# Kernel tuning notes

Measured on AMD Instinct MI355X. Metric: run time of the kernel, lower is better.

The kernel has to match this reference:

```python
import jax, jax.numpy as jnp
import numpy as np
from jax import lax

DEPTH = 8
LEAK = 0.01  # activations.relu(x, 0.01) == leaky relu


def _lrelu(z):
    return jnp.where(z >= 0, z, LEAK * z)


def _forward(x, mask, bucket_size, W_emb, b_emb, W, U, b, W1, b1,
             W_action_1, U_action_1, b_action_1, W_action_3, b_action_3):
    S = int(bucket_size)
    B = x.shape[0]
    H = W_emb.shape[1]
    dm = mask.T[:S]                         # [S,B] data mask (float)
    xe = x @ W_emb + b_emb                  # [B,S,H] embedding
    xe = jnp.transpose(xe, (1, 0, 2))[:S]   # [S,B,H] time-major
    # last_value_mask: 1 only at the final time step
    lvm = jnp.concatenate([jnp.zeros((S - 1, B), jnp.float32),
                           jnp.ones((1, B), jnp.float32)], axis=0)

    def hstep(carry, seq):
        h_tm1, nm_tm1, hv_tm1 = carry
        xt, pm, phv, lv = seq
        # action MLP -> per-sample gate
        a = _lrelu(xt @ W_action_1 + h_tm1 @ U_action_1 + b_action_1)  # [B,A]
        nm = jnp.clip(0.2 * (a @ W_action_3 + b_action_3) + 0.5, 0.0, 1.0)[:, 0]  # hard_sigmoid
        nm = (1.0 - lv) * (pm * phv * nm)
        both = pm * phv * (1.0 - nm) * hv_tm1
        x_only = pm * phv * (nm + (1.0 - nm) * (1.0 - hv_tm1))
        h_only = (1.0 - pm + pm * (1.0 - phv)) * (1.0 - nm) * hv_tm1
        hv = both + x_only + h_only
        h_ = _lrelu(xt @ W + h_tm1 @ U + b)      # [B,inner]
        h_ = _lrelu(h_ @ W1 + b1)                # [B,H]
        h = both[:, None] * h_ + x_only[:, None] * xt + h_only[:, None] * h_tm1
        return (h, nm, hv), (h, nm, hv)

    def vstep(carry, _):
        xv, xm, phv = carry  # [S,B,H], [S,B], [S,B]
        init = (jnp.zeros((B, H), jnp.float32),
                jnp.ones((B,), jnp.float32),
                jnp.zeros((B,), jnp.float32))
        _, (hs, nms, hvs) = lax.scan(hstep, init, (xv, xm, phv, lvm))
        # shift new_mask left by one step, pad last step with ones
        nms = jnp.concatenate([nms[1:], jnp.ones((1, B), jnp.float32)], axis=0)
        return (hs, nms, hvs), None

    (hfin, _, _), _ = lax.scan(vstep, (xe, dm, dm), None, length=DEPTH - 1)
    return hfin[-1]  # [B,H]: last time step of the last vertical level


def setup_inputs() -> dict:
    key = jax.random.key(0)
    ks = jax.random.split(key, 9)
    B, S, IN, H, INNER, A = 64, 256, 256, 256, 512, 64
    g = lambda k, shp: jax.random.normal(k, shp, jnp.float32) * np.float32(np.sqrt(2.0 / (shp[0] + shp[1])))
    return {
        "x": jax.random.normal(ks[0], (B, S, IN), jnp.float32),
        "mask": jnp.ones((B, S), jnp.float32),
        "bucket_size": S,
        "W_emb": g(ks[1], (IN, H)),
        "b_emb": jnp.zeros((H,), jnp.float32),
        "W": g(ks[2], (H, INNER)),
        "U": g(ks[3], (H, INNER)),
        "b": jnp.zeros((INNER,), jnp.float32),
        "W1": g(ks[4], (INNER, H)),
        "b1": jnp.zeros((H,), jnp.float32),
        "W_action_1": g(ks[5], (H, A)),
        "U_action_1": g(ks[6], (H, A)),
        "b_action_1": jnp.zeros((A,), jnp.float32),
        "W_action_3": g(ks[7], (A, 1)),
        "b_action_3": jnp.zeros((1,), jnp.float32),
    }


def reference(x, mask, bucket_size, W_emb, b_emb, W, U, b, W1, b1,
              W_action_1, U_action_1, b_action_1, W_action_3, b_action_3):
    return _forward(x, mask, bucket_size, W_emb, b_emb, W, U, b, W1, b1,
                    W_action_1, U_action_1, b_action_1, W_action_3, b_action_3)
```

## Files before the change

kernel.cpp:

```cpp
#include <hip/hip_runtime.h>
#include <stdint.h>


typedef _Float16 f16x8 __attribute__((ext_vector_type(8)));
typedef float    f32x4 __attribute__((ext_vector_type(4)));

static constexpr int SS = 256, BB = 64, DIN = 256, DH = 256, DNN = 512, DA = 64;

static constexpr size_t OFF_FLAGS = 0;
static constexpr size_t OFF_WEMB  = 8192;
static constexpr size_t SZ_WEMB   = (size_t)DIN * DH * 2;
static constexpr size_t OFF_W     = OFF_WEMB + SZ_WEMB;
static constexpr size_t SZ_WU     = (size_t)DH * DNN * 2;
static constexpr size_t OFF_U     = OFF_W + SZ_WU;
static constexpr size_t OFF_W1    = OFF_U + SZ_WU;
static constexpr size_t SZ_W1     = (size_t)DNN * DH * 2;
static constexpr size_t OFF_WA1   = OFF_W1 + SZ_W1;
static constexpr size_t SZ_WA     = (size_t)DH * DA * 2;
static constexpr size_t OFF_UA1   = OFF_WA1 + SZ_WA;
static constexpr size_t OFF_NM    = OFF_UA1 + SZ_WA;
static constexpr size_t SZ_NM     = (size_t)SS * BB * 4;
static constexpr size_t OFF_HV    = OFF_NM + 8 * SZ_NM;
static constexpr size_t OFF_G1    = OFF_HV + 8 * SZ_NM;
static constexpr size_t SZ_G1     = (size_t)BB * DNN * 2;
static constexpr size_t OFF_Z     = OFF_G1 + 8 * SZ_G1;
static constexpr size_t OFF_HB    = (size_t)4 << 20;
static constexpr size_t SZ_HB     = (size_t)SS * BB * DH * 2;
static constexpr size_t WS_NEEDED = OFF_HB + 8 * SZ_HB;

__device__ __forceinline__ float lrelu(float v) { return v >= 0.0f ? v : 0.01f * v; }

__device__ __forceinline__ f32x4 ld128(const f32x4* p) {
  f32x4 r;
  asm volatile("global_load_dwordx4 %0, %1, off sc0 sc1" : "=v"(r) : "v"(p) : "memory");
  return r;
}
__device__ __forceinline__ void st128(f32x4* p, f32x4 v) {
  asm volatile("global_store_dwordx4 %0, %1, off sc0 sc1" :: "v"(p), "v"(v) : "memory");
}
__device__ __forceinline__ float ldf(const float* p) {
  float r;
  asm volatile("global_load_dword %0, %1, off sc0 sc1" : "=v"(r) : "v"(p) : "memory");
  return r;
}
__device__ __forceinline__ void stf(float* p, float v) {
  asm volatile("global_store_dword %0, %1, off sc0 sc1" :: "v"(p), "v"(v) : "memory");
}
__device__ __forceinline__ void vwait() { asm volatile("s_waitcnt vmcnt(0)" ::: "memory"); }

__device__ __forceinline__ void pollf(const unsigned* p, unsigned need) {
  #pragma nounroll
  for (int g = 0; g < (1 << 18); ++g) {
    unsigned v;
    asm volatile("global_load_dword %0, %1, off sc0 sc1\n\ts_waitcnt vmcnt(0)"
                 : "=v"(v) : "v"(p) : "memory");
    if (v >= need) return;
  }
}

__global__ void zero_flags_k(unsigned* f) {
  f[threadIdx.x] = 0u;
  f[threadIdx.x + 1024] = 0u;
}

__global__ void pack_weight_k(const float* __restrict__ src, _Float16* __restrict__ dst,
                              int K, int N) {
  int idx = blockIdx.x * 256 + threadIdx.x;
  if (idx >= K * N) return;
  int k = idx / N, n = idx - k * N;
  int kt = k >> 5, q = (k >> 3) & 3, jj = k & 7;
  int nt = n >> 4, l = n & 15;
  size_t p = (((size_t)(kt * (N >> 4) + nt) * 4 + q) * 16 + l) * 8 + jj;
  dst[p] = (_Float16)src[idx];
}

__global__ __launch_bounds__(512, 2) void emb_k(const float* __restrict__ xin,
                                                const float* __restrict__ b_emb,
                                                char* __restrict__ ws) {
  const int tid = threadIdx.x, wave = tid >> 6, lane = tid & 63;
  const int l15 = lane & 15, quad = lane >> 4;
  const _Float16* Wp = (const _Float16*)(ws + OFF_WEMB);
  _Float16* xe = (_Float16*)(ws + OFF_HB);

  f16x8 bE[16];
  #pragma unroll
  for (int kt = 0; kt < 8; ++kt)
    #pragma unroll
    for (int i = 0; i < 2; ++i)
      bE[kt * 2 + i] = *(const f16x8*)(Wp + (((size_t)(kt * 16 + (wave * 2 + i)) * 4 + quad) * 16 + l15) * 8);
  float ber[2] = { b_emb[(wave * 2) * 16 + l15], b_emb[(wave * 2 + 1) * 16 + l15] };

  __shared__ __align__(16) _Float16 xtF[32 * 65 * 8];
  __shared__ __align__(16) _Float16 oF[32 * 65 * 8];

  for (int tt = 0; tt < 4; ++tt) {
    const int t = (int)blockIdx.x + 64 * tt;
    #pragma unroll
    for (int c = 0; c < 4; ++c) {
      int u = tid + 512 * c, s = u >> 5, kg = u & 31;
      const float* src = xin + ((size_t)s * SS + t) * DIN + kg * 8;
      f32x4 v0 = *(const f32x4*)src, v1 = *(const f32x4*)(src + 4);
      f16x8 p;
      p[0]=(_Float16)v0[0]; p[1]=(_Float16)v0[1]; p[2]=(_Float16)v0[2]; p[3]=(_Float16)v0[3];
      p[4]=(_Float16)v1[0]; p[5]=(_Float16)v1[1]; p[6]=(_Float16)v1[2]; p[7]=(_Float16)v1[3];
      *(f16x8*)(xtF + ((size_t)kg * 65 + s) * 8) = p;
    }
    __syncthreads();
    f32x4 acc[2][4] = {};
    #pragma unroll
    for (int kt = 0; kt < 8; ++kt) {
      f16x8 ax[4];
      #pragma unroll
      for (int mt = 0; mt < 4; ++mt)
        ax[mt] = *(const f16x8*)(xtF + (((size_t)(kt * 4 + quad)) * 65 + (mt * 16 + l15)) * 8);
      #pragma unroll
      for (int i = 0; i < 2; ++i)
        #pragma unroll
        for (int mt = 0; mt < 4; ++mt)
          acc[i][mt] = __builtin_amdgcn_mfma_f32_16x16x32_f16(ax[mt], bE[kt * 2 + i], acc[i][mt], 0, 0, 0);
    }
    #pragma unroll
    for (int i = 0; i < 2; ++i) {
      int n = (wave * 2 + i) * 16 + l15;
      int kq = n >> 3, jn = n & 7;
      #pragma unroll
      for (int mt = 0; mt < 4; ++mt)
        #pragma unroll
        for (int r = 0; r < 4; ++r) {
          int s = mt * 16 + quad * 4 + r;
          oF[((size_t)kq * 65 + s) * 8 + jn] = (_Float16)(acc[i][mt][r] + ber[i]);
        }
    }
    __syncthreads();
    #pragma unroll
    for (int c = 0; c < 4; ++c) {
      int u = tid + 512 * c, kq = u >> 6, s = u & 63;
      f32x4 v = *(const f32x4*)(oF + ((size_t)kq * 65 + s) * 8);
      *((f32x4*)(xe + (((size_t)t * 32 + kq) * 64 + s) * 8)) = v;
    }
    __syncthreads();
  }
}

__global__ __launch_bounds__(512, 2) void pipe_k(
    const float* __restrict__ mask, const float* __restrict__ b_in,
    const float* __restrict__ b1v, const float* __restrict__ bA1,
    const float* __restrict__ WA3, const float* __restrict__ bA3,
    char* __restrict__ ws, float* __restrict__ outp) {
  const int level = 1 + ((int)blockIdx.x >> 3);
  const int j     = (int)blockIdx.x & 7;
  const int tid   = threadIdx.x, wave = tid >> 6, lane = tid & 63;
  const int l15   = lane & 15, quad = lane >> 4;

  unsigned* flags = (unsigned*)(ws + OFF_FLAGS);
  unsigned* hfl   = flags + level * 64;
  unsigned* hflP  = flags + (level - 1) * 64;
  unsigned* gfl   = flags + (8 + level) * 64;

  const _Float16* Wp   = (const _Float16*)(ws + OFF_W);
  const _Float16* Up   = (const _Float16*)(ws + OFF_U);
  const _Float16* W1p  = (const _Float16*)(ws + OFF_W1);
  const _Float16* WA1p = (const _Float16*)(ws + OFF_WA1);
  const _Float16* UA1p = (const _Float16*)(ws + OFF_UA1);

  const f32x4* hPrev4 = (const f32x4*)((_Float16*)(ws + OFF_HB) + (size_t)(level - 1) * SS * BB * DH);
  f32x4*       hOwn4  = (f32x4*)((_Float16*)(ws + OFF_HB) + (size_t)level * SS * BB * DH);
  f32x4*       g1g4   = (f32x4*)(ws + OFF_G1 + (size_t)level * SZ_G1);
  float*       zg     = (float*)(ws + OFF_Z + (size_t)level * 4096);
  float*       nmW    = (float*)(ws + OFF_NM + (size_t)level * SZ_NM);
  float*       hvW    = (float*)(ws + OFF_HV + (size_t)level * SZ_NM);
  const float* nmR    = (const float*)(ws + OFF_NM + (size_t)(level - 1) * SZ_NM);
  const float* hvR    = (const float*)(ws + OFF_HV + (size_t)(level - 1) * SZ_NM);

  const int ntG = j * 4 + (wave >> 1);
  const int m0  = (wave & 1) * 2;
  f16x8 bW[8], bU[8];
  #pragma unroll
  for (int kt = 0; kt < 8; ++kt) {
    bW[kt] = *(const f16x8*)(Wp + (((size_t)(kt * 32 + ntG) * 4 + quad) * 16 + l15) * 8);
    bU[kt] = *(const f16x8*)(Up + (((size_t)(kt * 32 + ntG) * 4 + quad) * 16 + l15) * 8);
  }
  const int nt1 = j * 2 + (wave & 1);
  const int mt1 = wave >> 1;
  f16x8 b1f[16];
  #pragma unroll
  for (int kt = 0; kt < 16; ++kt)
    b1f[kt] = *(const f16x8*)(W1p + (((size_t)(kt * 16 + nt1) * 4 + quad) * 16 + l15) * 8);

  const int nG = ntG * 16 + l15;
  const int nC = nt1 * 16 + l15;
  const float bir  = b_in[nG];
  const float b1r  = b1v[nC];
  const float wa3r = WA3[(j & 3) * 16 + l15];
  const float ba1r = bA1[(j & 3) * 16 + l15];
  const float bA3v = bA3[0];

  __shared__ __align__(16) _Float16 xtF[32 * 64 * 8];
  __shared__ __align__(16) _Float16 htF[32 * 64 * 8];
  __shared__ __align__(16) _Float16 g1F[64 * 64 * 8];
  __shared__ __align__(16) _Float16 waF[16 * 64 * 8];
  __shared__ float gB[64], gX[64], gH[64], gHv[64];

  if (j < 4) {
    for (int u = tid; u < 1024; u += 512) {
      int ktm = u >> 6, lu = u & 63, kt = ktm >> 1, m = ktm & 1;
      const _Float16* sp = (m ? UA1p : WA1p) +
          (((size_t)(kt * 4 + j) * 4 + (lu >> 4)) * 16 + (lu & 15)) * 8;
      *(f16x8*)(waF + (size_t)u * 8) = *(const f16x8*)sp;
    }
  }
  for (int i = tid; i < 32 * 64 * 8; i += 512) htF[i] = (_Float16)0;
  if (tid < 64) gHv[tid] = 0.0f;
  float hreg[4] = {0.f, 0.f, 0.f, 0.f};
  __syncthreads();

  if (level >= 2) pollf(hflP + wave, 1);
  __syncthreads();
  {
    f32x4 pf[4];
    #pragma unroll
    for (int c = 0; c < 4; ++c) pf[c] = ld128(hPrev4 + tid + 512 * c);
    vwait();
    #pragma unroll
    for (int c = 0; c < 4; ++c) ((f32x4*)xtF)[tid + 512 * c] = pf[c];
  }
  __syncthreads();

  for (int t = 0; t < SS; ++t) {
    const bool last = (t == SS - 1);

    if (t > 0) pollf(hfl + wave, (unsigned)t);
    if (level >= 2) {
      unsigned need = (unsigned)((t + 2 <= SS) ? (t + 2) : SS);
      pollf(hflP + wave, need);
    }
    if (t > 0 && wave != j) {
      const f32x4* src = hOwn4 + (size_t)(t - 1) * 2048 + wave * 256;
      f32x4 hv4[4];
      #pragma unroll
      for (int it = 0; it < 4; ++it) hv4[it] = ld128(src + it * 64 + lane);
      vwait();
      #pragma unroll
      for (int it = 0; it < 4; ++it) ((f32x4*)htF)[wave * 256 + it * 64 + lane] = hv4[it];
    }
    __syncthreads();

    {
      f32x4 a0 = {}, a1 = {};
      #pragma unroll
      for (int kt = 0; kt < 8; ++kt) {
        int kq = kt * 4 + quad;
        f16x8 ax0 = *(const f16x8*)(xtF + ((size_t)(kq * 64 + m0 * 16 + l15)) * 8);
        f16x8 ax1 = *(const f16x8*)(xtF + ((size_t)(kq * 64 + (m0 + 1) * 16 + l15)) * 8);
        f16x8 ah0 = *(const f16x8*)(htF + ((size_t)(kq * 64 + m0 * 16 + l15)) * 8);
        f16x8 ah1 = *(const f16x8*)(htF + ((size_t)(kq * 64 + (m0 + 1) * 16 + l15)) * 8);
        a0 = __builtin_amdgcn_mfma_f32_16x16x32_f16(ax0, bW[kt], a0, 0, 0, 0);
        a1 = __builtin_amdgcn_mfma_f32_16x16x32_f16(ax1, bW[kt], a1, 0, 0, 0);
        a0 = __builtin_amdgcn_mfma_f32_16x16x32_f16(ah0, bU[kt], a0, 0, 0, 0);
        a1 = __builtin_amdgcn_mfma_f32_16x16x32_f16(ah1, bU[kt], a1, 0, 0, 0);
      }
      const int kqn = nG >> 3, jn = nG & 7;
      #pragma unroll
      for (int r = 0; r < 4; ++r) {
        g1F[((size_t)kqn * 64 + (m0 * 16 + quad * 4 + r)) * 8 + jn]       = (_Float16)lrelu(a0[r] + bir);
        g1F[((size_t)kqn * 64 + ((m0 + 1) * 16 + quad * 4 + r)) * 8 + jn] = (_Float16)lrelu(a1[r] + bir);
      }
      if (j < 4 && wave < 4) {
        f32x4 aa = {};
        #pragma unroll
        for (int kt = 0; kt < 8; ++kt) {
          int kq = kt * 4 + quad;
          f16x8 ax = *(const f16x8*)(xtF + ((size_t)(kq * 64 + wave * 16 + l15)) * 8);
          f16x8 ah = *(const f16x8*)(htF + ((size_t)(kq * 64 + wave * 16 + l15)) * 8);
          f16x8 bWa = *(const f16x8*)(waF + ((size_t)(kt * 2) * 64 + lane) * 8);
          f16x8 bUa = *(const f16x8*)(waF + ((size_t)(kt * 2 + 1) * 64 + lane) * 8);
          aa = __builtin_amdgcn_mfma_f32_16x16x32_f16(ax, bWa, aa, 0, 0, 0);
          aa = __builtin_amdgcn_mfma_f32_16x16x32_f16(ah, bUa, aa, 0, 0, 0);
        }
        #pragma unroll
        for (int r = 0; r < 4; ++r) {
          float v = lrelu(aa[r] + ba1r) * wa3r;
          v += __shfl_xor(v, 1); v += __shfl_xor(v, 2);
          v += __shfl_xor(v, 4); v += __shfl_xor(v, 8);
          if (l15 == 0) stf(&zg[j * 64 + wave * 16 + quad * 4 + r], v);
        }
      }
    }
    __syncthreads();
    {
      f32x4 v = ((const f32x4*)g1F)[j * 512 + tid];
      st128(g1g4 + j * 512 + tid, v);
      vwait();
    }
    __syncthreads();
    if (tid == 0)
      __hip_atomic_store(gfl + j, (unsigned)(t + 1), __ATOMIC_RELEASE, __HIP_MEMORY_SCOPE_AGENT);

    f32x4 pf[4];
    if (!last) {
      const f32x4* xs = hPrev4 + (size_t)(t + 1) * 2048;
      #pragma unroll
      for (int c = 0; c < 4; ++c) pf[c] = ld128(xs + tid + 512 * c);
      vwait();
    }

    if (wave != j) {
      pollf(gfl + wave, (unsigned)(t + 1));
      const f32x4* src = g1g4 + wave * 512;
      f32x4 g4[8];
      #pragma unroll
      for (int it = 0; it < 8; ++it) g4[it] = ld128(src + it * 64 + lane);
      vwait();
      #pragma unroll
      for (int it = 0; it < 8; ++it) ((f32x4*)g1F)[wave * 512 + it * 64 + lane] = g4[it];
    }
    __syncthreads();

    if (tid < 64) {
      int s = tid;
      float z0 = ldf(zg + s), z1 = ldf(zg + 64 + s), z2 = ldf(zg + 128 + s), z3 = ldf(zg + 192 + s);
      float pm, phv;
      if (level == 1) {
        vwait();
        float mv = mask[(size_t)s * SS + t];
        pm = mv; phv = mv;
      } else {
        size_t tn = (t + 1 < SS) ? (size_t)(t + 1) : 0;
        float pmv = ldf(nmR + tn * BB + s);
        float ph  = ldf(hvR + (size_t)t * BB + s);
        vwait();
        pm  = (t + 1 < SS) ? pmv : 1.0f;
        phv = ph;
      }
      float z    = bA3v + z0 + z1 + z2 + z3;
      float nm0  = fminf(fmaxf(0.2f * z + 0.5f, 0.0f), 1.0f);
      float lv   = last ? 1.0f : 0.0f;
      float nm   = (1.0f - lv) * (pm * phv * nm0);
      float hvp  = gHv[s], omn = 1.0f - nm;
      float both = pm * phv * omn * hvp;
      float xo   = pm * phv * (nm + omn * (1.0f - hvp));
      float ho   = (1.0f - pm * phv) * omn * hvp;
      float hv   = both + xo + ho;
      gB[s] = both; gX[s] = xo; gH[s] = ho; gHv[s] = hv;
      if (j == 0 && level < 7) {
        stf(&nmW[(size_t)t * BB + s], nm);
        stf(&hvW[(size_t)t * BB + s], hv);
      }
    }
    f32x4 c1 = {};
    #pragma unroll
    for (int kt = 0; kt < 16; ++kt) {
      f16x8 ag = *(const f16x8*)(g1F + ((size_t)((kt * 4 + quad) * 64 + mt1 * 16 + l15)) * 8);
      c1 = __builtin_amdgcn_mfma_f32_16x16x32_f16(ag, b1f[kt], c1, 0, 0, 0);
    }
    __syncthreads();

    {
      const int kqc = nC >> 3, jc = nC & 7;
      #pragma unroll
      for (int r = 0; r < 4; ++r) {
        int s = mt1 * 16 + quad * 4 + r;
        float h1  = lrelu(c1[r] + b1r);
        float xtv = (float)xtF[((size_t)(kqc * 64 + s)) * 8 + jc];
        float hn  = gB[s] * h1 + gX[s] * xtv + gH[s] * hreg[r];
        hreg[r] = hn;
        htF[((size_t)(kqc * 64 + s)) * 8 + jc] = (_Float16)hn;
        if (level == 7 && last) outp[(size_t)s * DH + nC] = hn;
      }
    }
    __syncthreads();
    if (tid < 256) {
      f32x4 v = ((const f32x4*)htF)[j * 256 + tid];
      st128(hOwn4 + (size_t)t * 2048 + j * 256 + tid, v);
    }
    if (!last) {
      #pragma unroll
      for (int c = 0; c < 4; ++c) ((f32x4*)xtF)[tid + 512 * c] = pf[c];
    }
    vwait();
    __syncthreads();
    if (tid == 0)
      __hip_atomic_store(hfl + j, (unsigned)(t + 1), __ATOMIC_RELEASE, __HIP_MEMORY_SCOPE_AGENT);
  }
}

extern "C" void kernel_launch(void* const* d_in, const int* in_sizes, int n_in,
                              void* d_out, int out_size, void* d_ws, size_t ws_size,
                              hipStream_t stream) {
  const float* x     = (const float*)d_in[0];
  const float* mask  = (const float*)d_in[1];
  const float* W_emb = (const float*)d_in[3];
  const float* b_emb = (const float*)d_in[4];
  const float* W     = (const float*)d_in[5];
  const float* U     = (const float*)d_in[6];
  const float* b     = (const float*)d_in[7];
  const float* W1    = (const float*)d_in[8];
  const float* b1    = (const float*)d_in[9];
  const float* WA1   = (const float*)d_in[10];
  const float* UA1   = (const float*)d_in[11];
  const float* bA1   = (const float*)d_in[12];
  const float* WA3   = (const float*)d_in[13];
  const float* bA3   = (const float*)d_in[14];
  char* ws = (char*)d_ws;

  if (ws_size < WS_NEEDED) return;

  zero_flags_k<<<1, 1024, 0, stream>>>((unsigned*)(ws + OFF_FLAGS));
  pack_weight_k<<<(DIN * DH + 255) / 256, 256, 0, stream>>>(W_emb, (_Float16*)(ws + OFF_WEMB), DIN, DH);
  pack_weight_k<<<(DH * DNN + 255) / 256, 256, 0, stream>>>(W, (_Float16*)(ws + OFF_W), DH, DNN);
  pack_weight_k<<<(DH * DNN + 255) / 256, 256, 0, stream>>>(U, (_Float16*)(ws + OFF_U), DH, DNN);
  pack_weight_k<<<(DNN * DH + 255) / 256, 256, 0, stream>>>(W1, (_Float16*)(ws + OFF_W1), DNN, DH);
  pack_weight_k<<<(DH * DA + 255) / 256, 256, 0, stream>>>(WA1, (_Float16*)(ws + OFF_WA1), DH, DA);
  pack_weight_k<<<(DH * DA + 255) / 256, 256, 0, stream>>>(UA1, (_Float16*)(ws + OFF_UA1), DH, DA);

  emb_k<<<64, 512, 0, stream>>>(x, b_emb, ws);
  pipe_k<<<56, 512, 0, stream>>>(mask, b, b1, bA1, WA3, bA3, ws, (float*)d_out);
}
```

Before: 3.598 ms.

## Restructure recurrent pipeline to make the full hidden state local and cut cross-block syncs

Each block now computes the entire W1 projection for all 256 hidden columns, with the first GEMM split over two K halves reduced through LDS. Every block therefore holds the full h_t locally, and the per-step exchange of hidden slices between the 8 blocks of a level goes away. Only the g1 activations and the action logits are still exchanged, through double-buffered global scratch, so one global flag handshake per step is removed. The next x_t is prefetched with global_load_lds DMA into ping-pong LDS buffers, and the mask is pre-transposed for coalesced loads. In exchange each block does 8x redundant W1 MFMA work and holds more registers, which adds compute and register pressure.

```diff
diff --git a/kernel.cpp b/kernel.cpp
--- a/kernel.cpp
+++ b/kernel.cpp
@@ -4,26 +4,24 @@
 
 typedef _Float16 f16x8 __attribute__((ext_vector_type(8)));
 typedef float    f32x4 __attribute__((ext_vector_type(4)));
+typedef unsigned int u32;
 
 static constexpr int SS = 256, BB = 64, DIN = 256, DH = 256, DNN = 512, DA = 64;
 
 static constexpr size_t OFF_FLAGS = 0;
-static constexpr size_t OFF_WEMB  = 8192;
-static constexpr size_t SZ_WEMB   = (size_t)DIN * DH * 2;
-static constexpr size_t OFF_W     = OFF_WEMB + SZ_WEMB;
-static constexpr size_t SZ_WU     = (size_t)DH * DNN * 2;
-static constexpr size_t OFF_U     = OFF_W + SZ_WU;
-static constexpr size_t OFF_W1    = OFF_U + SZ_WU;
-static constexpr size_t SZ_W1     = (size_t)DNN * DH * 2;
-static constexpr size_t OFF_WA1   = OFF_W1 + SZ_W1;
-static constexpr size_t SZ_WA     = (size_t)DH * DA * 2;
-static constexpr size_t OFF_UA1   = OFF_WA1 + SZ_WA;
-static constexpr size_t OFF_NM    = OFF_UA1 + SZ_WA;
+static constexpr size_t OFF_MASKT = 8192;
+static constexpr size_t OFF_WEMB  = OFF_MASKT + 65536;
+static constexpr size_t OFF_W     = OFF_WEMB + (size_t)DIN * DH * 2;
+static constexpr size_t OFF_U     = OFF_W + (size_t)DH * DNN * 2;
+static constexpr size_t OFF_W1    = OFF_U + (size_t)DH * DNN * 2;
+static constexpr size_t OFF_WA1   = OFF_W1 + (size_t)DNN * DH * 2;
+static constexpr size_t OFF_UA1   = OFF_WA1 + (size_t)DH * DA * 2;
+static constexpr size_t OFF_NM    = OFF_UA1 + (size_t)DH * DA * 2;
 static constexpr size_t SZ_NM     = (size_t)SS * BB * 4;
 static constexpr size_t OFF_HV    = OFF_NM + 8 * SZ_NM;
 static constexpr size_t OFF_G1    = OFF_HV + 8 * SZ_NM;
 static constexpr size_t SZ_G1     = (size_t)BB * DNN * 2;
-static constexpr size_t OFF_Z     = OFF_G1 + 8 * SZ_G1;
+static constexpr size_t OFF_Z     = OFF_G1 + 8 * 2 * SZ_G1;
 static constexpr size_t OFF_HB    = (size_t)4 << 20;
 static constexpr size_t SZ_HB     = (size_t)SS * BB * DH * 2;
 static constexpr size_t WS_NEEDED = OFF_HB + 8 * SZ_HB;
@@ -46,21 +44,41 @@
 __device__ __forceinline__ void stf(float* p, float v) {
   asm volatile("global_store_dword %0, %1, off sc0 sc1" :: "v"(p), "v"(v) : "memory");
 }
+__device__ __forceinline__ void stu(u32* p, u32 v) {
+  asm volatile("global_store_dword %0, %1, off sc0 sc1" :: "v"(p), "v"(v) : "memory");
+}
+__device__ __forceinline__ u32 ldu(const u32* p) {
+  u32 r;
+  asm volatile("global_load_dword %0, %1, off sc0 sc1\n\ts_waitcnt vmcnt(0)"
+               : "=v"(r) : "v"(p) : "memory");
+  return r;
+}
 __device__ __forceinline__ void vwait() { asm volatile("s_waitcnt vmcnt(0)" ::: "memory"); }
 
-__device__ __forceinline__ void pollf(const unsigned* p, unsigned need) {
+__device__ __forceinline__ void poll1(const u32* p, u32 need) {
   #pragma nounroll
-  for (int g = 0; g < (1 << 18); ++g) {
-    unsigned v;
-    asm volatile("global_load_dword %0, %1, off sc0 sc1\n\ts_waitcnt vmcnt(0)"
-                 : "=v"(v) : "v"(p) : "memory");
-    if (v >= need) return;
-  }
-}
-
-__global__ void zero_flags_k(unsigned* f) {
-  f[threadIdx.x] = 0u;
-  f[threadIdx.x + 1024] = 0u;
+  for (int g = 0; g < (1 << 17); ++g) { if (ldu(p) >= need) return; }
+}
+__device__ __forceinline__ void poll8(const u32* base, u32 need, int lane) {
+  #pragma nounroll
+  for (int g = 0; g < (1 << 17); ++g) {
+    u32 v = ldu(base + (lane & 7));
+    if (__all((int)(v >= need))) return;
+  }
+}
+
+__device__ __forceinline__ void dma16(const _Float16* g, _Float16* l) {
+  auto* gp = (const __attribute__((address_space(1))) u32*)(uintptr_t)g;
+  auto* lp = (__attribute__((address_space(3))) u32*)(uintptr_t)l;
+  __builtin_amdgcn_global_load_lds(gp, lp, 16, 0, 0);
+}
+
+__global__ void zero_flags_k(u32* f) { f[threadIdx.x] = 0u; f[threadIdx.x + 1024] = 0u; }
+
+__global__ void maskT_k(const float* __restrict__ mask, float* __restrict__ mT) {
+  int idx = blockIdx.x * 256 + threadIdx.x;
+  int t = idx >> 6, s = idx & 63;
+  mT[idx] = mask[(size_t)s * SS + t];
 }
 
 __global__ void pack_weight_k(const float* __restrict__ src, _Float16* __restrict__ dst,
@@ -143,62 +161,63 @@
 }
 
 __global__ __launch_bounds__(512, 2) void pipe_k(
-    const float* __restrict__ mask, const float* __restrict__ b_in,
-    const float* __restrict__ b1v, const float* __restrict__ bA1,
-    const float* __restrict__ WA3, const float* __restrict__ bA3,
-    char* __restrict__ ws, float* __restrict__ outp) {
+    const float* __restrict__ b_in, const float* __restrict__ b1v,
+    const float* __restrict__ bA1, const float* __restrict__ WA3,
+    const float* __restrict__ bA3, char* __restrict__ ws,
+    float* __restrict__ outp) {
   const int level = 1 + ((int)blockIdx.x >> 3);
   const int j     = (int)blockIdx.x & 7;
   const int tid   = threadIdx.x, wave = tid >> 6, lane = tid & 63;
   const int l15   = lane & 15, quad = lane >> 4;
-
-  unsigned* flags = (unsigned*)(ws + OFF_FLAGS);
-  unsigned* hfl   = flags + level * 64;
-  unsigned* hflP  = flags + (level - 1) * 64;
-  unsigned* gfl   = flags + (8 + level) * 64;
+  const int khalf = wave >> 2, ntL = wave & 3;
+
+  u32* flags = (u32*)(ws + OFF_FLAGS);
+  u32* gfl   = flags + level * 16;
+  u32* hfl   = flags + 256 + level * 16;
+  u32* hflP  = flags + 256 + (level - 1) * 16;
 
   const _Float16* Wp   = (const _Float16*)(ws + OFF_W);
   const _Float16* Up   = (const _Float16*)(ws + OFF_U);
   const _Float16* W1p  = (const _Float16*)(ws + OFF_W1);
   const _Float16* WA1p = (const _Float16*)(ws + OFF_WA1);
   const _Float16* UA1p = (const _Float16*)(ws + OFF_UA1);
-
-  const f32x4* hPrev4 = (const f32x4*)((_Float16*)(ws + OFF_HB) + (size_t)(level - 1) * SS * BB * DH);
-  f32x4*       hOwn4  = (f32x4*)((_Float16*)(ws + OFF_HB) + (size_t)level * SS * BB * DH);
-  f32x4*       g1g4   = (f32x4*)(ws + OFF_G1 + (size_t)level * SZ_G1);
-  float*       zg     = (float*)(ws + OFF_Z + (size_t)level * 4096);
-  float*       nmW    = (float*)(ws + OFF_NM + (size_t)level * SZ_NM);
-  float*       hvW    = (float*)(ws + OFF_HV + (size_t)level * SZ_NM);
-  const float* nmR    = (const float*)(ws + OFF_NM + (size_t)(level - 1) * SZ_NM);
-  const float* hvR    = (const float*)(ws + OFF_HV + (size_t)(level - 1) * SZ_NM);
-
-  const int ntG = j * 4 + (wave >> 1);
-  const int m0  = (wave & 1) * 2;
-  f16x8 bW[8], bU[8];
+  const float*    maskT = (const float*)(ws + OFF_MASKT);
+
+  const _Float16* xsrc = (const _Float16*)(ws + OFF_HB) + (size_t)(level - 1) * SS * BB * DH;
+  _Float16* hdst = (level < 7) ? (_Float16*)(ws + OFF_HB) + (size_t)level * SS * BB * DH : nullptr;
+  _Float16* g1g  = (_Float16*)(ws + OFF_G1) + (size_t)level * 2 * BB * DNN;
+  float*    zg   = (float*)(ws + OFF_Z) + (size_t)level * 512;
+  float*    nmW  = (float*)(ws + OFF_NM + (size_t)level * SZ_NM);
+  float*    hvW  = (float*)(ws + OFF_HV + (size_t)level * SZ_NM);
+  const float* nmR = (const float*)(ws + OFF_NM + (size_t)(level - 1) * SZ_NM);
+  const float* hvR = (const float*)(ws + OFF_HV + (size_t)(level - 1) * SZ_NM);
+
+  f16x8 bW[4], bU[4];
   #pragma unroll
-  for (int kt = 0; kt < 8; ++kt) {
-    bW[kt] = *(const f16x8*)(Wp + (((size_t)(kt * 32 + ntG) * 4 + quad) * 16 + l15) * 8);
-    bU[kt] = *(const f16x8*)(Up + (((size_t)(kt * 32 + ntG) * 4 + quad) * 16 + l15) * 8);
-  }
-  const int nt1 = j * 2 + (wave & 1);
-  const int mt1 = wave >> 1;
-  f16x8 b1f[16];
+  for (int i = 0; i < 4; ++i) {
+    int kt = khalf * 4 + i;
+    bW[i] = *(const f16x8*)(Wp + (((size_t)(kt * 32 + j * 4 + ntL) * 4 + quad) * 16 + l15) * 8);
+    bU[i] = *(const f16x8*)(Up + (((size_t)(kt * 32 + j * 4 + ntL) * 4 + quad) * 16 + l15) * 8);
+  }
+  f16x8 b1f[2][16];
   #pragma unroll
-  for (int kt = 0; kt < 16; ++kt)
-    b1f[kt] = *(const f16x8*)(W1p + (((size_t)(kt * 16 + nt1) * 4 + quad) * 16 + l15) * 8);
-
-  const int nG = ntG * 16 + l15;
-  const int nC = nt1 * 16 + l15;
-  const float bir  = b_in[nG];
-  const float b1r  = b1v[nC];
+  for (int h2 = 0; h2 < 2; ++h2)
+    #pragma unroll
+    for (int kt = 0; kt < 16; ++kt)
+      b1f[h2][kt] = *(const f16x8*)(W1p + (((size_t)(kt * 16 + wave * 2 + h2) * 4 + quad) * 16 + l15) * 8);
+
+  const float birD = b_in[j * 64 + ntL * 16 + l15];
+  const float b1r0 = b1v[(wave * 2) * 16 + l15];
+  const float b1r1 = b1v[(wave * 2 + 1) * 16 + l15];
+  const float ba1r = bA1[(j & 3) * 16 + l15];
   const float wa3r = WA3[(j & 3) * 16 + l15];
-  const float ba1r = bA1[(j & 3) * 16 + l15];
   const float bA3v = bA3[0];
 
-  __shared__ __align__(16) _Float16 xtF[32 * 64 * 8];
-  __shared__ __align__(16) _Float16 htF[32 * 64 * 8];
+  __shared__ __align__(16) _Float16 bufA[32 * 64 * 8];
+  __shared__ __align__(16) _Float16 bufB[32 * 64 * 8];
   __shared__ __align__(16) _Float16 g1F[64 * 64 * 8];
   __shared__ __align__(16) _Float16 waF[16 * 64 * 8];
+  __shared__ float zarr[256], nmA[64], hvA[64];
   __shared__ float gB[64], gX[64], gH[64], gHv[64];
 
   if (j < 4) {
@@ -209,178 +228,191 @@
       *(f16x8*)(waF + (size_t)u * 8) = *(const f16x8*)sp;
     }
   }
-  for (int i = tid; i < 32 * 64 * 8; i += 512) htF[i] = (_Float16)0;
+  #pragma unroll
+  for (int c = 0; c < 4; ++c) ((f32x4*)bufB)[tid + 512 * c] = f32x4{0.f, 0.f, 0.f, 0.f};
   if (tid < 64) gHv[tid] = 0.0f;
-  float hreg[4] = {0.f, 0.f, 0.f, 0.f};
+  float hreg[2][4][4] = {};
+
+  if (level >= 2 && wave == 0) poll8(hflP, 1, lane);
   __syncthreads();
-
-  if (level >= 2) pollf(hflP + wave, 1);
+  #pragma unroll
+  for (int c = 0; c < 4; ++c) {
+    int ub = wave * 256 + c * 64;
+    dma16(xsrc + (size_t)(ub + lane) * 8, bufA + (size_t)ub * 8);
+  }
+  vwait();
   __syncthreads();
-  {
-    f32x4 pf[4];
-    #pragma unroll
-    for (int c = 0; c < 4; ++c) pf[c] = ld128(hPrev4 + tid + 512 * c);
-    vwait();
-    #pragma unroll
-    for (int c = 0; c < 4; ++c) ((f32x4*)xtF)[tid + 512 * c] = pf[c];
-  }
-  __syncthreads();
 
   for (int t = 0; t < SS; ++t) {
-    const bool last = (t == SS - 1);
-
-    if (t > 0) pollf(hfl + wave, (unsigned)t);
-    if (level >= 2) {
-      unsigned need = (unsigned)((t + 2 <= SS) ? (t + 2) : SS);
-      pollf(hflP + wave, need);
-    }
-    if (t > 0 && wave != j) {
-      const f32x4* src = hOwn4 + (size_t)(t - 1) * 2048 + wave * 256;
-      f32x4 hv4[4];
-      #pragma unroll
-      for (int it = 0; it < 4; ++it) hv4[it] = ld128(src + it * 64 + lane);
-      vwait();
-      #pragma unroll
-      for (int it = 0; it < 4; ++it) ((f32x4*)htF)[wave * 256 + it * 64 + lane] = hv4[it];
-    }
-    __syncthreads();
-
+    const int par = t & 1;
+    _Float16* bufX = par ? bufB : bufA;
+    _Float16* bufH = par ? bufA : bufB;
+    _Float16* g1p  = g1g + (size_t)par * BB * DNN;
+    float*    zp   = zg + par * 256;
+
+    f32x4 dacc[4] = {};
+    f32x4 aacc = {0.f, 0.f, 0.f, 0.f};
+    #pragma unroll
+    for (int i = 0; i < 4; ++i) {
+      int kq = (khalf * 4 + i) * 4 + quad;
+      f16x8 ax[4], ah[4];
+      #pragma unroll
+      for (int mt = 0; mt < 4; ++mt) {
+        ax[mt] = *(const f16x8*)(bufX + ((size_t)kq * 64 + mt * 16 + l15) * 8);
+        ah[mt] = *(const f16x8*)(bufH + ((size_t)kq * 64 + mt * 16 + l15) * 8);
+      }
+      #pragma unroll
+      for (int mt = 0; mt < 4; ++mt) {
+        dacc[mt] = __builtin_amdgcn_mfma_f32_16x16x32_f16(ax[mt], bW[i], dacc[mt], 0, 0, 0);
+        dacc[mt] = __builtin_amdgcn_mfma_f32_16x16x32_f16(ah[mt], bU[i], dacc[mt], 0, 0, 0);
+      }
+      if (j < 4) {
+        f16x8 bWa = *(const f16x8*)(waF + ((size_t)((khalf * 4 + i) * 2) * 64 + lane) * 8);
+        f16x8 bUa = *(const f16x8*)(waF + ((size_t)((khalf * 4 + i) * 2 + 1) * 64 + lane) * 8);
+        aacc = __builtin_amdgcn_mfma_f32_16x16x32_f16(ax[ntL], bWa, aacc, 0, 0, 0);
+        aacc = __builtin_amdgcn_mfma_f32_16x16x32_f16(ah[ntL], bUa, aacc, 0, 0, 0);
+      }
+    }
     {
-      f32x4 a0 = {}, a1 = {};
-      #pragma unroll
-      for (int kt = 0; kt < 8; ++kt) {
-        int kq = kt * 4 + quad;
-        f16x8 ax0 = *(const f16x8*)(xtF + ((size_t)(kq * 64 + m0 * 16 + l15)) * 8);
-        f16x8 ax1 = *(const f16x8*)(xtF + ((size_t)(kq * 64 + (m0 + 1) * 16 + l15)) * 8);
-        f16x8 ah0 = *(const f16x8*)(htF + ((size_t)(kq * 64 + m0 * 16 + l15)) * 8);
-        f16x8 ah1 = *(const f16x8*)(htF + ((size_t)(kq * 64 + (m0 + 1) * 16 + l15)) * 8);
-        a0 = __builtin_amdgcn_mfma_f32_16x16x32_f16(ax0, bW[kt], a0, 0, 0, 0);
-        a1 = __builtin_amdgcn_mfma_f32_16x16x32_f16(ax1, bW[kt], a1, 0, 0, 0);
-        a0 = __builtin_amdgcn_mfma_f32_16x16x32_f16(ah0, bU[kt], a0, 0, 0, 0);
-        a1 = __builtin_amdgcn_mfma_f32_16x16x32_f16(ah1, bU[kt], a1, 0, 0, 0);
-      }
-      const int kqn = nG >> 3, jn = nG & 7;
-      #pragma unroll
-      for (int r = 0; r < 4; ++r) {
-        g1F[((size_t)kqn * 64 + (m0 * 16 + quad * 4 + r)) * 8 + jn]       = (_Float16)lrelu(a0[r] + bir);
-        g1F[((size_t)kqn * 64 + ((m0 + 1) * 16 + quad * 4 + r)) * 8 + jn] = (_Float16)lrelu(a1[r] + bir);
-      }
-      if (j < 4 && wave < 4) {
-        f32x4 aa = {};
-        #pragma unroll
-        for (int kt = 0; kt < 8; ++kt) {
-          int kq = kt * 4 + quad;
-          f16x8 ax = *(const f16x8*)(xtF + ((size_t)(kq * 64 + wave * 16 + l15)) * 8);
-          f16x8 ah = *(const f16x8*)(htF + ((size_t)(kq * 64 + wave * 16 + l15)) * 8);
-          f16x8 bWa = *(const f16x8*)(waF + ((size_t)(kt * 2) * 64 + lane) * 8);
-          f16x8 bUa = *(const f16x8*)(waF + ((size_t)(kt * 2 + 1) * 64 + lane) * 8);
-          aa = __builtin_amdgcn_mfma_f32_16x16x32_f16(ax, bWa, aa, 0, 0, 0);
-          aa = __builtin_amdgcn_mfma_f32_16x16x32_f16(ah, bUa, aa, 0, 0, 0);
+      f32x4* scr = (f32x4*)g1F;
+      const int slotWU = ((j + 1 + (ntL >> 1)) & 7);
+      if (khalf) {
+        #pragma unroll
+        for (int mt = 0; mt < 4; ++mt)
+          scr[slotWU * 512 + (ntL & 1) * 256 + mt * 64 + lane] = dacc[mt];
+        if (j < 4) scr[((j + 3) & 7) * 512 + ntL * 64 + lane] = aacc;
+      }
+      __syncthreads();
+      if (!khalf) {
+        const int n = j * 64 + ntL * 16 + l15, kqG = n >> 3, jn = n & 7;
+        #pragma unroll
+        for (int mt = 0; mt < 4; ++mt) {
+          f32x4 o = scr[slotWU * 512 + (ntL & 1) * 256 + mt * 64 + lane];
+          #pragma unroll
+          for (int r = 0; r < 4; ++r) {
+            float g = lrelu(dacc[mt][r] + o[r] + birD);
+            g1F[((size_t)kqG * 64 + mt * 16 + quad * 4 + r) * 8 + jn] = (_Float16)g;
+          }
         }
-        #pragma unroll
-        for (int r = 0; r < 4; ++r) {
-          float v = lrelu(aa[r] + ba1r) * wa3r;
-          v += __shfl_xor(v, 1); v += __shfl_xor(v, 2);
-          v += __shfl_xor(v, 4); v += __shfl_xor(v, 8);
-          if (l15 == 0) stf(&zg[j * 64 + wave * 16 + quad * 4 + r], v);
+        if (j < 4) {
+          f32x4 o = scr[((j + 3) & 7) * 512 + ntL * 64 + lane];
+          #pragma unroll
+          for (int r = 0; r < 4; ++r) {
+            float a = lrelu(aacc[r] + o[r] + ba1r) * wa3r;
+            a += __shfl_xor(a, 1); a += __shfl_xor(a, 2);
+            a += __shfl_xor(a, 4); a += __shfl_xor(a, 8);
+            if (l15 == 0) zarr[j * 64 + ntL * 16 + quad * 4 + r] = a;
+          }
         }
       }
     }
     __syncthreads();
+
     {
       f32x4 v = ((const f32x4*)g1F)[j * 512 + tid];
-      st128(g1g4 + j * 512 + tid, v);
+      st128((f32x4*)g1p + j * 512 + tid, v);
+      if (j < 4 && tid < 64) stf(zp + j * 64 + tid, zarr[j * 64 + tid]);
+    }
+    vwait();
+    __syncthreads();
+    if (tid == 0) stu(gfl + j, (u32)(t + 1));
+
+    if (wave != j) {
+      poll1(gfl + wave, (u32)(t + 1));
+      const f32x4* src = (const f32x4*)g1p + wave * 512;
+      f32x4 g4[8];
+      #pragma unroll
+      for (int it = 0; it < 8; ++it) g4[it] = ld128(src + it * 64 + lane);
+      float zv = 0.0f;
+      if (wave < 4) zv = ldf(zp + wave * 64 + lane);
       vwait();
-    }
-    __syncthreads();
-    if (tid == 0)
-      __hip_atomic_store(gfl + j, (unsigned)(t + 1), __ATOMIC_RELEASE, __HIP_MEMORY_SCOPE_AGENT);
-
-    f32x4 pf[4];
-    if (!last) {
-      const f32x4* xs = hPrev4 + (size_t)(t + 1) * 2048;
-      #pragma unroll
-      for (int c = 0; c < 4; ++c) pf[c] = ld128(xs + tid + 512 * c);
-      vwait();
-    }
-
-    if (wave != j) {
-      pollf(gfl + wave, (unsigned)(t + 1));
-      const f32x4* src = g1g4 + wave * 512;
-      f32x4 g4[8];
-      #pragma unroll
-      for (int it = 0; it < 8; ++it) g4[it] = ld128(src + it * 64 + lane);
-      vwait();
       #pragma unroll
       for (int it = 0; it < 8; ++it) ((f32x4*)g1F)[wave * 512 + it * 64 + lane] = g4[it];
-    }
-    __syncthreads();
-
-    if (tid < 64) {
-      int s = tid;
-      float z0 = ldf(zg + s), z1 = ldf(zg + 64 + s), z2 = ldf(zg + 128 + s), z3 = ldf(zg + 192 + s);
-      float pm, phv;
-      if (level == 1) {
+      if (wave < 4) zarr[wave * 64 + lane] = zv;
+    } else {
+      if (level >= 2) {
+        u32 need = (u32)((t + 2 <= SS) ? (t + 2) : SS);
+        poll8(hflP, need, lane);
+        float nmv = ldf(nmR + (size_t)((t + 1 < SS) ? (t + 1) : (SS - 1)) * 64 + lane);
+        float hvv = ldf(hvR + (size_t)t * 64 + lane);
         vwait();
-        float mv = mask[(size_t)s * SS + t];
-        pm = mv; phv = mv;
+        nmA[lane] = nmv; hvA[lane] = hvv;
       } else {
-        size_t tn = (t + 1 < SS) ? (size_t)(t + 1) : 0;
-        float pmv = ldf(nmR + tn * BB + s);
-        float ph  = ldf(hvR + (size_t)t * BB + s);
-        vwait();
-        pm  = (t + 1 < SS) ? pmv : 1.0f;
-        phv = ph;
-      }
-      float z    = bA3v + z0 + z1 + z2 + z3;
-      float nm0  = fminf(fmaxf(0.2f * z + 0.5f, 0.0f), 1.0f);
-      float lv   = last ? 1.0f : 0.0f;
-      float nm   = (1.0f - lv) * (pm * phv * nm0);
-      float hvp  = gHv[s], omn = 1.0f - nm;
+        float mv = maskT[(size_t)t * 64 + lane];
+        nmA[lane] = mv; hvA[lane] = mv;
+      }
+    }
+    __syncthreads();
+
+    if (t + 1 < SS) {
+      const _Float16* src = xsrc + (size_t)(t + 1) * BB * DH;
+      #pragma unroll
+      for (int c = 0; c < 4; ++c) {
+        int ub = wave * 256 + c * 64;
+        dma16(src + (size_t)(ub + lane) * 8, bufH + (size_t)ub * 8);
+      }
+    }
+    if (wave == 0) {
+      int s = lane;
+      float z   = bA3v + zarr[s] + zarr[64 + s] + zarr[128 + s] + zarr[192 + s];
+      float nm0 = fminf(fmaxf(0.2f * z + 0.5f, 0.0f), 1.0f);
+      float pm  = (level >= 2 && t + 1 >= SS) ? 1.0f : nmA[s];
+      float phv = hvA[s];
+      float lv  = (t == SS - 1) ? 1.0f : 0.0f;
+      float nm  = (1.0f - lv) * (pm * phv * nm0);
+      float hvp = gHv[s], omn = 1.0f - nm;
       float both = pm * phv * omn * hvp;
       float xo   = pm * phv * (nm + omn * (1.0f - hvp));
       float ho   = (1.0f - pm * phv) * omn * hvp;
       float hv   = both + xo + ho;
       gB[s] = both; gX[s] = xo; gH[s] = ho; gHv[s] = hv;
-      if (j == 0 && level < 7) {
-        stf(&nmW[(size_t)t * BB + s], nm);
-        stf(&hvW[(size_t)t * BB + s], hv);
-      }
-    }
-    f32x4 c1 = {};
+      if (level < 7) {
+        stf(nmW + (size_t)t * 64 + s, nm);
+        stf(hvW + (size_t)t * 64 + s, hv);
+      }
+    }
+    __syncthreads();
+
+    f32x4 c1[2][4] = {};
     #pragma unroll
     for (int kt = 0; kt < 16; ++kt) {
-      f16x8 ag = *(const f16x8*)(g1F + ((size_t)((kt * 4 + quad) * 64 + mt1 * 16 + l15)) * 8);
-      c1 = __builtin_amdgcn_mfma_f32_16x16x32_f16(ag, b1f[kt], c1, 0, 0, 0);
-    }
-    __syncthreads();
-
-    {
-      const int kqc = nC >> 3, jc = nC & 7;
-      #pragma unroll
-      for (int r = 0; r < 4; ++r) {
-        int s = mt1 * 16 + quad * 4 + r;
-        float h1  = lrelu(c1[r] + b1r);
-        float xtv = (float)xtF[((size_t)(kqc * 64 + s)) * 8 + jc];
-        float hn  = gB[s] * h1 + gX[s] * xtv + gH[s] * hreg[r];
-        hreg[r] = hn;
-        htF[((size_t)(kqc * 64 + s)) * 8 + jc] = (_Float16)hn;
-        if (level == 7 && last) outp[(size_t)s * DH + nC] = hn;
-      }
-    }
-    __syncthreads();
-    if (tid < 256) {
-      f32x4 v = ((const f32x4*)htF)[j * 256 + tid];
-      st128(hOwn4 + (size_t)t * 2048 + j * 256 + tid, v);
-    }
-    if (!last) {
-      #pragma unroll
-      for (int c = 0; c < 4; ++c) ((f32x4*)xtF)[tid + 512 * c] = pf[c];
+      int kq = kt * 4 + quad;
+      f16x8 ag[4];
+      #pragma unroll
+      for (int mt = 0; mt < 4; ++mt)
+        ag[mt] = *(const f16x8*)(g1F + ((size_t)kq * 64 + mt * 16 + l15) * 8);
+      #pragma unroll
+      for (int h2 = 0; h2 < 2; ++h2)
+        #pragma unroll
+        for (int mt = 0; mt < 4; ++mt)
+          c1[h2][mt] = __builtin_amdgcn_mfma_f32_16x16x32_f16(ag[mt], b1f[h2][kt], c1[h2][mt], 0, 0, 0);
+    }
+    #pragma unroll
+    for (int h2 = 0; h2 < 2; ++h2) {
+      const int n = (wave * 2 + h2) * 16 + l15, kqc = n >> 3, jc = n & 7;
+      const float b1r = h2 ? b1r1 : b1r0;
+      #pragma unroll
+      for (int mt = 0; mt < 4; ++mt)
+        #pragma unroll
+        for (int r = 0; r < 4; ++r) {
+          int s = mt * 16 + quad * 4 + r;
+          float h1  = lrelu(c1[h2][mt][r] + b1r);
+          float xtv = (float)bufX[((size_t)kqc * 64 + s) * 8 + jc];
+          float hn  = gB[s] * h1 + gX[s] * xtv + gH[s] * hreg[h2][mt][r];
+          hreg[h2][mt][r] = hn;
+          bufX[((size_t)kqc * 64 + s) * 8 + jc] = (_Float16)hn;
+          if (level == 7 && t == SS - 1) outp[(size_t)s * DH + n] = hn;
+        }
+    }
+    __syncthreads();
+
+    if (level < 7 && tid < 256) {
+      f32x4 v = ((const f32x4*)bufX)[j * 256 + tid];
+      st128((f32x4*)(hdst + (size_t)t * BB * DH) + j * 256 + tid, v);
     }
     vwait();
     __syncthreads();
-    if (tid == 0)
-      __hip_atomic_store(hfl + j, (unsigned)(t + 1), __ATOMIC_RELEASE, __HIP_MEMORY_SCOPE_AGENT);
+    if (level < 7 && tid == 0) stu(hfl + j, (u32)(t + 1));
   }
 }
 
@@ -405,7 +437,8 @@
 
   if (ws_size < WS_NEEDED) return;
 
-  zero_flags_k<<<1, 1024, 0, stream>>>((unsigned*)(ws + OFF_FLAGS));
+  zero_flags_k<<<1, 1024, 0, stream>>>((u32*)(ws + OFF_FLAGS));
+  maskT_k<<<64, 256, 0, stream>>>(mask, (float*)(ws + OFF_MASKT));
   pack_weight_k<<<(DIN * DH + 255) / 256, 256, 0, stream>>>(W_emb, (_Float16*)(ws + OFF_WEMB), DIN, DH);
   pack_weight_k<<<(DH * DNN + 255) / 256, 256, 0, stream>>>(W, (_Float16*)(ws + OFF_W), DH, DNN);
   pack_weight_k<<<(DH * DNN + 255) / 256, 256, 0, stream>>>(U, (_Float16*)(ws + OFF_U), DH, DNN);
@@ -414,5 +447,5 @@
   pack_weight_k<<<(DH * DA + 255) / 256, 256, 0, stream>>>(UA1, (_Float16*)(ws + OFF_UA1), DH, DA);
 
   emb_k<<<64, 512, 0, stream>>>(x, b_emb, ws);
-  pipe_k<<<56, 512, 0, stream>>>(mask, b, b1, bA1, WA3, bA3, ws, (float*)d_out);
-}
+  pipe_k<<<56, 512, 0, stream>>>(b, b1, bA1, WA3, bA3, ws, (float*)d_out);
+}
```

Result: slower. 11.29 ms (+213.9%).
